# Optimization experiments

Hardware: AMD Instinct MI355X
Metric: run time of the kernel (lower is better)

Reference implementation:

```python
import jax, jax.numpy as jnp
import numpy as np

B, T, D, H = 4, 2048, 512, 8
K = D // H  # head dim = 64

def setup_inputs() -> dict:
    key = jax.random.key(0)
    k1, k2, k3, k4 = jax.random.split(key, 4)
    x = jax.random.normal(k1, (B, T, D), dtype=jnp.float32)
    # torch nn.Linear stores weight as [out_features, in_features]
    w_qkv = jax.random.normal(k2, (3 * D, D), dtype=jnp.float32) * (D ** -0.5)
    w_proj = jax.random.normal(k3, (D, D), dtype=jnp.float32) * (D ** -0.5)
    b_proj = jax.random.normal(k4, (D,), dtype=jnp.float32) * 0.01
    return {"x": x, "w_qkv": w_qkv, "w_proj": w_proj, "b_proj": b_proj}

def reference(x, w_qkv, w_proj, b_proj):
    Bx, Tx, Dx = x.shape
    # qkv projection (no bias): [B,T,3D]
    qkv = jnp.einsum('btd,ed->bte', x, w_qkv)
    q, k, v = jnp.split(qkv, 3, axis=-1)
    # [B,H,T,K]
    def heads(t):
        return t.reshape(Bx, Tx, H, K).transpose(0, 2, 1, 3)
    q, k, v = heads(q), heads(k), heads(v)
    # scaled scores with causal mask
    scores = jnp.einsum('bhqk,bhsk->bhqs', q, k) * (K ** -0.5)  # [B,H,T,T]
    causal = jnp.tril(jnp.ones((Tx, Tx), dtype=bool))
    scores = jnp.where(causal, scores, -jnp.inf)
    attn = jax.nn.softmax(scores, axis=-1)  # dropout p=0.0 -> identity
    out = jnp.einsum('bhqs,bhsk->bhqk', attn, v)  # [B,H,T,K]
    out = out.transpose(0, 2, 1, 3).reshape(Bx, Tx, Dx)
    out = jnp.einsum('btd,ed->bte', out, w_proj) + b_proj
    return out
```

## Files before the change

### kernel.cpp

```cpp
#include <hip/hip_runtime.h>
#include <hip/hip_bf16.h>


typedef unsigned short u16;
typedef __attribute__((ext_vector_type(8))) __bf16 bf16x8;
typedef __attribute__((ext_vector_type(8))) unsigned short u16x8;
typedef __attribute__((ext_vector_type(4))) unsigned short u16x4;
typedef __attribute__((ext_vector_type(4))) float f32x4;
typedef __attribute__((ext_vector_type(4))) unsigned u32x4;
typedef __attribute__((ext_vector_type(2))) unsigned u32x2;

#define DEV static __device__ __forceinline__

DEV void async16(const u16* g, u16* l) {
  __builtin_amdgcn_global_load_lds(
      (const __attribute__((address_space(1))) unsigned int*)g,
      (__attribute__((address_space(3))) unsigned int*)l, 16, 0, 0);
}
DEV u16x8 gld8(const u16* p) { return *(const u16x8*)p; }
DEV void lst8(u16* p, u16x8 v) { *(u16x8*)p = v; }
DEV bf16x8 ldsld8(const u16* p) {
  return __builtin_bit_cast(bf16x8, *(const u16x8*)p);
}
DEV f32x4 mfma16(bf16x8 a, bf16x8 b, f32x4 c) {
  return __builtin_amdgcn_mfma_f32_16x16x32_bf16(a, b, c, 0, 0, 0);
}
DEV u16 f2b(float f) {
  unsigned u = __builtin_bit_cast(unsigned, f);
  u += 0x7FFFu + ((u >> 16) & 1u);
  return (u16)(u >> 16);
}
DEV unsigned pk2(float x, float y) {
  __hip_bfloat162 t = __float22bfloat162_rn(float2{x, y});
  unsigned r;
  __builtin_memcpy(&r, &t, 4);
  return r;
}
DEV u16x8 pack8(f32x4 a, f32x4 b) {
  u32x4 t;
  t[0] = pk2(a[0], a[1]);
  t[1] = pk2(a[2], a[3]);
  t[2] = pk2(b[0], b[1]);
  t[3] = pk2(b[2], b[3]);
  return __builtin_bit_cast(u16x8, t);
}

__global__ void cvt_all(const float* __restrict__ x, const float* __restrict__ wq,
                        u16* __restrict__ xb, u16* __restrict__ wqb) {
  constexpr long NX = 8192L * 512 / 8;
  constexpr long NQ = 1536L * 512 / 8;
  const long i = (long)blockIdx.x * 256 + threadIdx.x;
  if (i < NX) {
    const float* p = x + i * 8;
    *(u16x8*)(xb + i * 8) = pack8(*(const f32x4*)p, *(const f32x4*)(p + 4));
  } else if (i < NX + NQ) {
    const long j = i - NX;
    const float* p = wq + j * 8;
    *(u16x8*)(wqb + j * 8) = pack8(*(const f32x4*)p, *(const f32x4*)(p + 4));
  }
}

__global__ void gemm_bb(const u16* __restrict__ A, const u16* __restrict__ Bt,
                        u16* __restrict__ qk, u16* __restrict__ vT, int K) {
  __shared__ __align__(16) u16 As[2][128 * 32];
  __shared__ __align__(16) u16 Bs[2][128 * 32];

  const int t = threadIdx.x, lane = t & 63, w = t >> 6;
  const int lane15 = lane & 15, quad = lane >> 4;
  const int wr = w >> 1, wc = w & 1;

  const int i = blockIdx.x;
  const int rt = (i & 7) | (((i >> 3) & 7) << 3);
  const int ct = i >> 6;
  const long row0 = (long)rt * 128;
  const int col0 = ct * 128;

  const int srow = w * 16 + (lane >> 2);
  const int scol = (lane & 3) * 8;
  const u16* Ag = A + (row0 + srow) * (long)K + scol;
  const u16* Bg = Bt + ((long)col0 + srow) * (long)K + scol;

  f32x4 acc[4][4];
#pragma unroll
  for (int ii = 0; ii < 4; ii++)
#pragma unroll
    for (int j = 0; j < 4; j++) acc[ii][j] = (f32x4)(0.0f);

  for (int k0 = 0; k0 < K; k0 += 64) {
    __syncthreads();
#pragma unroll
    for (int r = 0; r < 2; r++)
#pragma unroll
      for (int hf = 0; hf < 2; hf++) {
        async16(Ag + (long)r * 64 * K + k0 + hf * 32,
                &As[hf][(r * 64 + w * 16) * 32]);
        async16(Bg + (long)r * 64 * K + k0 + hf * 32,
                &Bs[hf][(r * 64 + w * 16) * 32]);
      }
    __syncthreads();

#pragma unroll
    for (int hf = 0; hf < 2; hf++) {
      bf16x8 a[4], b[4];
#pragma unroll
      for (int ii = 0; ii < 4; ii++)
        a[ii] = ldsld8(&As[hf][(wr * 64 + ii * 16 + lane15) * 32 + quad * 8]);
#pragma unroll
      for (int j = 0; j < 4; j++)
        b[j] = ldsld8(&Bs[hf][(wc * 64 + j * 16 + lane15) * 32 + quad * 8]);
#pragma unroll
      for (int ii = 0; ii < 4; ii++)
#pragma unroll
        for (int j = 0; j < 4; j++) acc[ii][j] = mfma16(a[ii], b[j], acc[ii][j]);
    }
  }

  if (col0 >= 1024) {
#pragma unroll
    for (int ii = 0; ii < 4; ii++)
#pragma unroll
      for (int j = 0; j < 4; j++) {
        const int hd = col0 - 1024 + wc * 64 + j * 16 + lane15;
        const long row = row0 + wr * 64 + ii * 16 + quad * 4;
        const long bb = row >> 11;
        const int s = (int)(row & 2047);
        const int ps = (s & ~31) | (((s >> 2) & 3) << 3) | (((s >> 4) & 1) << 2);
        u32x2 pr;
        pr[0] = pk2(acc[ii][j][0], acc[ii][j][1]);
        pr[1] = pk2(acc[ii][j][2], acc[ii][j][3]);
        *(u16x4*)(vT + (bb * 512 + hd) * 2048 + ps) =
            __builtin_bit_cast(u16x4, pr);
      }
  } else {
#pragma unroll
    for (int ii = 0; ii < 4; ii++)
#pragma unroll
      for (int j = 0; j < 4; j++) {
        const int col = col0 + wc * 64 + j * 16 + lane15;
        const float sc = (col < 512) ? 0.18033688f : 1.0f;
#pragma unroll
        for (int r = 0; r < 4; r++) {
          const long row = row0 + wr * 64 + ii * 16 + quad * 4 + r;
          qk[row * 1024 + col] = f2b(acc[ii][j][r] * sc);
        }
      }
  }
}

__global__ void gemm_b64(const u16* __restrict__ A, const float* __restrict__ Bt,
                         const float* __restrict__ bias, float* __restrict__ C,
                         int N, int K) {
  __shared__ __align__(16) u16 As[2][128 * 32];
  __shared__ __align__(16) u16 Bs[2][64 * 32];

  const int t = threadIdx.x, lane = t & 63, w = t >> 6;
  const int lane15 = lane & 15, quad = lane >> 4;
  const int wr = w >> 1, wc = w & 1;

  const int i = blockIdx.x;
  const int rt = (i & 7) | (((i >> 3) & 7) << 3);
  const int ct = i >> 6;
  const long row0 = (long)rt * 128;
  const int col0 = ct * 64;

  const int srow = w * 16 + (lane >> 2);
  const int scol = (lane & 3) * 8;
  const u16* Ag = A + (row0 + srow) * (long)K + scol;

  const int brow = t >> 2, bc = (t & 3) * 16;
  const float* Bg = Bt + (long)(col0 + brow) * K + bc;
  u16* BsD = &Bs[bc >> 5][brow * 32 + (bc & 31)];

  f32x4 acc[4][2];
#pragma unroll
  for (int ii = 0; ii < 4; ii++)
#pragma unroll
    for (int j = 0; j < 2; j++) acc[ii][j] = (f32x4)(0.0f);

  f32x4 q0 = *(const f32x4*)Bg, q1 = *(const f32x4*)(Bg + 4);
  f32x4 q2 = *(const f32x4*)(Bg + 8), q3 = *(const f32x4*)(Bg + 12);

  for (int k0 = 0; k0 < K; k0 += 64) {
    __syncthreads();
#pragma unroll
    for (int r = 0; r < 2; r++)
#pragma unroll
      for (int hf = 0; hf < 2; hf++)
        async16(Ag + (long)r * 64 * K + k0 + hf * 32,
                &As[hf][(r * 64 + w * 16) * 32]);
    lst8(BsD, pack8(q0, q1));
    lst8(BsD + 8, pack8(q2, q3));
    __syncthreads();

    {
      const int kp = (k0 + 64 < K) ? k0 + 64 : k0;
      q0 = *(const f32x4*)(Bg + kp);     q1 = *(const f32x4*)(Bg + kp + 4);
      q2 = *(const f32x4*)(Bg + kp + 8); q3 = *(const f32x4*)(Bg + kp + 12);
    }

#pragma unroll
    for (int hf = 0; hf < 2; hf++) {
      bf16x8 a[4], b[2];
#pragma unroll
      for (int ii = 0; ii < 4; ii++)
        a[ii] = ldsld8(&As[hf][(wr * 64 + ii * 16 + lane15) * 32 + quad * 8]);
#pragma unroll
      for (int j = 0; j < 2; j++)
        b[j] = ldsld8(&Bs[hf][(wc * 32 + j * 16 + lane15) * 32 + quad * 8]);
#pragma unroll
      for (int ii = 0; ii < 4; ii++)
#pragma unroll
        for (int j = 0; j < 2; j++) acc[ii][j] = mfma16(a[ii], b[j], acc[ii][j]);
    }
  }

#pragma unroll
  for (int ii = 0; ii < 4; ii++)
#pragma unroll
    for (int j = 0; j < 2; j++) {
      const int col = col0 + wc * 32 + j * 16 + lane15;
      const float bv = bias[col];
#pragma unroll
      for (int r = 0; r < 4; r++) {
        const long row = row0 + wr * 64 + ii * 16 + quad * 4 + r;
        C[row * (long)N + col] = acc[ii][j][r] + bv;
      }
    }
}

__global__ void attn_v8(const u16* __restrict__ qk, const u16* __restrict__ vT,
                        u16* __restrict__ out) {
  constexpr int T = 2048, LDQ = 1024;
  __shared__ __align__(16) u16 Ks[2][64 * 72];
  __shared__ __align__(16) u16 Vs[2][64 * 72];

  const int t = threadIdx.x, lane = t & 63, w = t >> 6;
  const int lane15 = lane & 15, quad = lane >> 4;

  const int i = blockIdx.x;
  int qb = i & 15;
  if (i >= 256) qb = 15 - qb;
  const int h = (i >> 4) & 7;
  const int b = (i >> 7) & 3;
  const long baseq = (long)b * T * LDQ;
  const u16* vTb = vT + ((long)b * 512 + h * 64) * 2048;

  const u16* gq =
      qk + baseq + (long)(qb * 128 + w * 32 + lane15) * LDQ + h * 64 + quad * 8;
  const bf16x8 qa0 = __builtin_bit_cast(bf16x8, *(const u16x8*)gq);
  const bf16x8 qa1 = __builtin_bit_cast(bf16x8, *(const u16x8*)(gq + 32));
  const bf16x8 qc0 = __builtin_bit_cast(bf16x8, *(const u16x8*)(gq + 16 * LDQ));
  const bf16x8 qc1 =
      __builtin_bit_cast(bf16x8, *(const u16x8*)(gq + 16 * LDQ + 32));

  const int srow = t >> 3, sc8 = (t & 7) * 8;
  const int nsb = 2 * qb + 2;
  const int sbd = 2 * qb + (w >> 1);

  const u16* gk = qk + baseq + (long)srow * LDQ + 512 + h * 64 + sc8;
  const u16* gv = vTb + (long)srow * 2048 + sc8;

  u16x8 kr0, kr1, vr0, vr1;
  kr0 = gld8(gk); kr1 = gld8(gk + (long)32 * LDQ);
  vr0 = gld8(gv); vr1 = gld8(gv + (long)32 * 2048);
  lst8(&Ks[0][srow * 72 + sc8], kr0);
  lst8(&Ks[0][(srow + 32) * 72 + sc8], kr1);
  lst8(&Vs[0][srow * 72 + sc8], vr0);
  lst8(&Vs[0][(srow + 32) * 72 + sc8], vr1);
  gk += (long)64 * LDQ;
  gv += 64;
  kr0 = gld8(gk); kr1 = gld8(gk + (long)32 * LDQ);
  vr0 = gld8(gv); vr1 = gld8(gv + (long)32 * 2048);

  f32x4 o0[4], o1[4], lsum0 = (f32x4)(0.0f), lsum1 = (f32x4)(0.0f);
#pragma unroll
  for (int j = 0; j < 4; j++) { o0[j] = (f32x4)(0.0f); o1[j] = (f32x4)(0.0f); }

  const bf16x8 ones = __builtin_bit_cast(bf16x8, (u16x8)((u16)0x3F80));
  const int ql0 = ((w & 1) << 5) + lane15;

  for (int sb = 0; sb < nsb; ++sb) {
    const u16* Kc = Ks[sb & 1];
    const u16* Vc = Vs[sb & 1];
    u16* Kn = Ks[(sb + 1) & 1];
    u16* Vn = Vs[(sb + 1) & 1];

    __syncthreads();

    lst8(&Kn[srow * 72 + sc8], kr0);
    lst8(&Kn[(srow + 32) * 72 + sc8], kr1);
    lst8(&Vn[srow * 72 + sc8], vr0);
    lst8(&Vn[(srow + 32) * 72 + sc8], vr1);

    if (sb + 2 < nsb) { gk += (long)64 * LDQ; gv += 64; }
    kr0 = gld8(gk); kr1 = gld8(gk + (long)32 * LDQ);
    vr0 = gld8(gv); vr1 = gld8(gv + (long)32 * 2048);

    if (sb <= sbd) {
      __builtin_amdgcn_s_setprio(1);
      f32x4 s0[4], s1[4];
#pragma unroll
      for (int j = 0; j < 4; j++) {
        const bf16x8 k0 = ldsld8(&Kc[(j * 16 + lane15) * 72 + quad * 8]);
        const bf16x8 k1 = ldsld8(&Kc[(j * 16 + lane15) * 72 + quad * 8 + 32]);
        s0[j] = mfma16(k1, qa1, mfma16(k0, qa0, (f32x4)(0.0f)));
        s1[j] = mfma16(k1, qc1, mfma16(k0, qc0, (f32x4)(0.0f)));
      }

#pragma unroll
      for (int j = 0; j < 4; j++)
#pragma unroll
        for (int r = 0; r < 4; r++) {
          s0[j][r] = exp2f(s0[j][r]);
          s1[j][r] = exp2f(s1[j][r]);
        }
      if (sb == sbd) {
#pragma unroll
        for (int j = 0; j < 4; j++)
#pragma unroll
          for (int r = 0; r < 4; r++) {
            const int sl = j * 16 + quad * 4 + r;
            if (sl > ql0) s0[j][r] = 0.0f;
            if (sl > ql0 + 16) s1[j][r] = 0.0f;
          }
      }

      u32x4 w0, w1, w2, w3;
      w0[0] = pk2(s0[0][0], s0[0][1]); w0[1] = pk2(s0[0][2], s0[0][3]);
      w0[2] = pk2(s0[1][0], s0[1][1]); w0[3] = pk2(s0[1][2], s0[1][3]);
      w1[0] = pk2(s0[2][0], s0[2][1]); w1[1] = pk2(s0[2][2], s0[2][3]);
      w1[2] = pk2(s0[3][0], s0[3][1]); w1[3] = pk2(s0[3][2], s0[3][3]);
      w2[0] = pk2(s1[0][0], s1[0][1]); w2[1] = pk2(s1[0][2], s1[0][3]);
      w2[2] = pk2(s1[1][0], s1[1][1]); w2[3] = pk2(s1[1][2], s1[1][3]);
      w3[0] = pk2(s1[2][0], s1[2][1]); w3[1] = pk2(s1[2][2], s1[2][3]);
      w3[2] = pk2(s1[3][0], s1[3][1]); w3[3] = pk2(s1[3][2], s1[3][3]);
      const bf16x8 pa0 = __builtin_bit_cast(bf16x8, w0);
      const bf16x8 pa1 = __builtin_bit_cast(bf16x8, w1);
      const bf16x8 pc0 = __builtin_bit_cast(bf16x8, w2);
      const bf16x8 pc1 = __builtin_bit_cast(bf16x8, w3);

#pragma unroll
      for (int j = 0; j < 4; j++) {
        const int d0 = (j * 16 + lane15) * 72;
        const bf16x8 v0 = ldsld8(&Vc[d0 + quad * 8]);
        const bf16x8 v1 = ldsld8(&Vc[d0 + quad * 8 + 32]);
        o0[j] = mfma16(pa1, v1, mfma16(pa0, v0, o0[j]));
        o1[j] = mfma16(pc1, v1, mfma16(pc0, v0, o1[j]));
      }
      lsum0 = mfma16(pa1, ones, mfma16(pa0, ones, lsum0));
      lsum1 = mfma16(pc1, ones, mfma16(pc0, ones, lsum1));
      __builtin_amdgcn_s_setprio(0);
    }
  }

  const long orow0 = (long)b * T + qb * 128 + w * 32;
  f32x4 inv0, inv1;
#pragma unroll
  for (int r = 0; r < 4; r++) {
    inv0[r] = 1.0f / lsum0[r];
    inv1[r] = 1.0f / lsum1[r];
  }
#pragma unroll
  for (int j = 0; j < 4; j++)
#pragma unroll
    for (int r = 0; r < 4; r++) {
      const long rr = orow0 + quad * 4 + r;
      out[rr * 512 + h * 64 + j * 16 + lane15] = f2b(o0[j][r] * inv0[r]);
      out[(rr + 16) * 512 + h * 64 + j * 16 + lane15] = f2b(o1[j][r] * inv1[r]);
    }
}

extern "C" void kernel_launch(void* const* d_in, const int* in_sizes, int n_in,
                              void* d_out, int out_size, void* d_ws, size_t ws_size,
                              hipStream_t stream) {
  const float* x      = (const float*)d_in[0];
  const float* w_qkv  = (const float*)d_in[1];
  const float* w_proj = (const float*)d_in[2];
  const float* b_proj = (const float*)d_in[3];
  float* out = (float*)d_out;

  u16* qk = (u16*)d_ws;
  u16* vT = qk + (size_t)8192 * 1024;
  u16* xb = vT + (size_t)4 * 512 * 2048;
  u16* wqb = (u16*)d_out;

  cvt_all<<<2432, 256, 0, stream>>>(x, w_qkv, xb, wqb);
  gemm_bb<<<768, 256, 0, stream>>>(xb, wqb, qk, vT, 512);
  attn_v8<<<512, 256, 0, stream>>>(qk, vT, xb);
  gemm_b64<<<512, 256, 0, stream>>>(xb, w_proj, b_proj, out, 512, 512);
}
```

Measured before the change: 153.7 us.

## Split attention key range across two wave-halves per block and combine via LDS

The attention kernel now launches 512 threads per block, with two groups of 4 waves. Each group processes half of the causal key blocks for the same 128 query rows using its own double-buffered K/V LDS tiles. At the end, the second group writes its unnormalized partial outputs and row sums to LDS, and the first group adds them, normalizes and stores. This is meant to shorten the serial per-block key loop and raise wave count for the long-causal blocks, at the cost of doubled LDS, an extra combine step, and block-wide syncs that now span both halves.

```diff
diff --git a/kernel.cpp b/kernel.cpp
--- a/kernel.cpp
+++ b/kernel.cpp
@@ -228,14 +228,16 @@
     }
 }
 
-__global__ void attn_v8(const u16* __restrict__ qk, const u16* __restrict__ vT,
-                        u16* __restrict__ out) {
+__global__ void __launch_bounds__(512, 4)
+attn_v9(const u16* __restrict__ qk, const u16* __restrict__ vT,
+        u16* __restrict__ out) {
   constexpr int T = 2048, LDQ = 1024;
-  __shared__ __align__(16) u16 Ks[2][64 * 72];
-  __shared__ __align__(16) u16 Vs[2][64 * 72];
+  __shared__ __align__(16) u16 Ks[2][2][64 * 72];
+  __shared__ __align__(16) u16 Vs[2][2][64 * 72];
 
   const int t = threadIdx.x, lane = t & 63, w = t >> 6;
   const int lane15 = lane & 15, quad = lane >> 4;
+  const int half = w >> 2, wl = w & 3;
 
   const int i = blockIdx.x;
   int qb = i & 15;
@@ -246,29 +248,30 @@
   const u16* vTb = vT + ((long)b * 512 + h * 64) * 2048;
 
   const u16* gq =
-      qk + baseq + (long)(qb * 128 + w * 32 + lane15) * LDQ + h * 64 + quad * 8;
+      qk + baseq + (long)(qb * 128 + wl * 32 + lane15) * LDQ + h * 64 + quad * 8;
   const bf16x8 qa0 = __builtin_bit_cast(bf16x8, *(const u16x8*)gq);
   const bf16x8 qa1 = __builtin_bit_cast(bf16x8, *(const u16x8*)(gq + 32));
   const bf16x8 qc0 = __builtin_bit_cast(bf16x8, *(const u16x8*)(gq + 16 * LDQ));
   const bf16x8 qc1 =
       __builtin_bit_cast(bf16x8, *(const u16x8*)(gq + 16 * LDQ + 32));
 
-  const int srow = t >> 3, sc8 = (t & 7) * 8;
-  const int nsb = 2 * qb + 2;
-  const int sbd = 2 * qb + (w >> 1);
-
-  const u16* gk = qk + baseq + (long)srow * LDQ + 512 + h * 64 + sc8;
-  const u16* gv = vTb + (long)srow * 2048 + sc8;
+  const int th = t & 255;
+  const int srow = th >> 3, sc8 = (th & 7) * 8;
+  const int nsbh = qb + 1;
+  const int s0 = half * nsbh;
+  const int sbd = 2 * qb + (wl >> 1);
+
+  const u16* gk = qk + baseq + (long)(s0 * 64 + srow) * LDQ + 512 + h * 64 + sc8;
+  const u16* gv = vTb + (long)srow * 2048 + s0 * 64 + sc8;
 
   u16x8 kr0, kr1, vr0, vr1;
   kr0 = gld8(gk); kr1 = gld8(gk + (long)32 * LDQ);
   vr0 = gld8(gv); vr1 = gld8(gv + (long)32 * 2048);
-  lst8(&Ks[0][srow * 72 + sc8], kr0);
-  lst8(&Ks[0][(srow + 32) * 72 + sc8], kr1);
-  lst8(&Vs[0][srow * 72 + sc8], vr0);
-  lst8(&Vs[0][(srow + 32) * 72 + sc8], vr1);
-  gk += (long)64 * LDQ;
-  gv += 64;
+  lst8(&Ks[half][0][srow * 72 + sc8], kr0);
+  lst8(&Ks[half][0][(srow + 32) * 72 + sc8], kr1);
+  lst8(&Vs[half][0][srow * 72 + sc8], vr0);
+  lst8(&Vs[half][0][(srow + 32) * 72 + sc8], vr1);
+  if (nsbh > 1) { gk += (long)64 * LDQ; gv += 64; }
   kr0 = gld8(gk); kr1 = gld8(gk + (long)32 * LDQ);
   vr0 = gld8(gv); vr1 = gld8(gv + (long)32 * 2048);
 
@@ -277,13 +280,13 @@
   for (int j = 0; j < 4; j++) { o0[j] = (f32x4)(0.0f); o1[j] = (f32x4)(0.0f); }
 
   const bf16x8 ones = __builtin_bit_cast(bf16x8, (u16x8)((u16)0x3F80));
-  const int ql0 = ((w & 1) << 5) + lane15;
-
-  for (int sb = 0; sb < nsb; ++sb) {
-    const u16* Kc = Ks[sb & 1];
-    const u16* Vc = Vs[sb & 1];
-    u16* Kn = Ks[(sb + 1) & 1];
-    u16* Vn = Vs[(sb + 1) & 1];
+  const int ql0 = ((wl & 1) << 5) + lane15;
+
+  for (int it = 0; it < nsbh; ++it) {
+    const u16* Kc = Ks[half][it & 1];
+    const u16* Vc = Vs[half][it & 1];
+    u16* Kn = Ks[half][(it + 1) & 1];
+    u16* Vn = Vs[half][(it + 1) & 1];
 
     __syncthreads();
 
@@ -292,27 +295,28 @@
     lst8(&Vn[srow * 72 + sc8], vr0);
     lst8(&Vn[(srow + 32) * 72 + sc8], vr1);
 
-    if (sb + 2 < nsb) { gk += (long)64 * LDQ; gv += 64; }
+    if (it + 2 < nsbh) { gk += (long)64 * LDQ; gv += 64; }
     kr0 = gld8(gk); kr1 = gld8(gk + (long)32 * LDQ);
     vr0 = gld8(gv); vr1 = gld8(gv + (long)32 * 2048);
 
+    const int sb = s0 + it;
     if (sb <= sbd) {
       __builtin_amdgcn_s_setprio(1);
-      f32x4 s0[4], s1[4];
+      f32x4 sf0[4], sf1[4];
 #pragma unroll
       for (int j = 0; j < 4; j++) {
         const bf16x8 k0 = ldsld8(&Kc[(j * 16 + lane15) * 72 + quad * 8]);
         const bf16x8 k1 = ldsld8(&Kc[(j * 16 + lane15) * 72 + quad * 8 + 32]);
-        s0[j] = mfma16(k1, qa1, mfma16(k0, qa0, (f32x4)(0.0f)));
-        s1[j] = mfma16(k1, qc1, mfma16(k0, qc0, (f32x4)(0.0f)));
+        sf0[j] = mfma16(k1, qa1, mfma16(k0, qa0, (f32x4)(0.0f)));
+        sf1[j] = mfma16(k1, qc1, mfma16(k0, qc0, (f32x4)(0.0f)));
       }
 
 #pragma unroll
       for (int j = 0; j < 4; j++)
 #pragma unroll
         for (int r = 0; r < 4; r++) {
-          s0[j][r] = exp2f(s0[j][r]);
-          s1[j][r] = exp2f(s1[j][r]);
+          sf0[j][r] = exp2f(sf0[j][r]);
+          sf1[j][r] = exp2f(sf1[j][r]);
         }
       if (sb == sbd) {
 #pragma unroll
@@ -320,20 +324,20 @@
 #pragma unroll
           for (int r = 0; r < 4; r++) {
             const int sl = j * 16 + quad * 4 + r;
-            if (sl > ql0) s0[j][r] = 0.0f;
-            if (sl > ql0 + 16) s1[j][r] = 0.0f;
+            if (sl > ql0) sf0[j][r] = 0.0f;
+            if (sl > ql0 + 16) sf1[j][r] = 0.0f;
           }
       }
 
       u32x4 w0, w1, w2, w3;
-      w0[0] = pk2(s0[0][0], s0[0][1]); w0[1] = pk2(s0[0][2], s0[0][3]);
-      w0[2] = pk2(s0[1][0], s0[1][1]); w0[3] = pk2(s0[1][2], s0[1][3]);
-      w1[0] = pk2(s0[2][0], s0[2][1]); w1[1] = pk2(s0[2][2], s0[2][3]);
-      w1[2] = pk2(s0[3][0], s0[3][1]); w1[3] = pk2(s0[3][2], s0[3][3]);
-      w2[0] = pk2(s1[0][0], s1[0][1]); w2[1] = pk2(s1[0][2], s1[0][3]);
-      w2[2] = pk2(s1[1][0], s1[1][1]); w2[3] = pk2(s1[1][2], s1[1][3]);
-      w3[0] = pk2(s1[2][0], s1[2][1]); w3[1] = pk2(s1[2][2], s1[2][3]);
-      w3[2] = pk2(s1[3][0], s1[3][1]); w3[3] = pk2(s1[3][2], s1[3][3]);
+      w0[0] = pk2(sf0[0][0], sf0[0][1]); w0[1] = pk2(sf0[0][2], sf0[0][3]);
+      w0[2] = pk2(sf0[1][0], sf0[1][1]); w0[3] = pk2(sf0[1][2], sf0[1][3]);
+      w1[0] = pk2(sf0[2][0], sf0[2][1]); w1[1] = pk2(sf0[2][2], sf0[2][3]);
+      w1[2] = pk2(sf0[3][0], sf0[3][1]); w1[3] = pk2(sf0[3][2], sf0[3][3]);
+      w2[0] = pk2(sf1[0][0], sf1[0][1]); w2[1] = pk2(sf1[0][2], sf1[0][3]);
+      w2[2] = pk2(sf1[1][0], sf1[1][1]); w2[3] = pk2(sf1[1][2], sf1[1][3]);
+      w3[0] = pk2(sf1[2][0], sf1[2][1]); w3[1] = pk2(sf1[2][2], sf1[2][3]);
+      w3[2] = pk2(sf1[3][0], sf1[3][1]); w3[3] = pk2(sf1[3][2], sf1[3][3]);
       const bf16x8 pa0 = __builtin_bit_cast(bf16x8, w0);
       const bf16x8 pa1 = __builtin_bit_cast(bf16x8, w1);
       const bf16x8 pc0 = __builtin_bit_cast(bf16x8, w2);
@@ -353,21 +357,49 @@
     }
   }
 
-  const long orow0 = (long)b * T + qb * 128 + w * 32;
-  f32x4 inv0, inv1;
-#pragma unroll
-  for (int r = 0; r < 4; r++) {
-    inv0[r] = 1.0f / lsum0[r];
-    inv1[r] = 1.0f / lsum1[r];
-  }
-#pragma unroll
-  for (int j = 0; j < 4; j++)
+  __syncthreads();
+  float* cmb = (float*)&Ks[0][0][0];
+  float* cl = (float*)&Vs[0][0][0];
+
+  if (half == 1) {
+    const int q0 = wl * 32 + quad * 4;
+#pragma unroll
+    for (int j = 0; j < 4; j++)
+#pragma unroll
+      for (int r = 0; r < 4; r++) {
+        cmb[(q0 + r) * 64 + j * 16 + lane15] = o0[j][r];
+        cmb[(q0 + 16 + r) * 64 + j * 16 + lane15] = o1[j][r];
+      }
+    if (lane15 == 0) {
+#pragma unroll
+      for (int r = 0; r < 4; r++) {
+        cl[q0 + r] = lsum0[r];
+        cl[q0 + 16 + r] = lsum1[r];
+      }
+    }
+  }
+  __syncthreads();
+
+  if (half == 0) {
+    const int q0 = wl * 32 + quad * 4;
+    f32x4 inv0, inv1;
 #pragma unroll
     for (int r = 0; r < 4; r++) {
-      const long rr = orow0 + quad * 4 + r;
-      out[rr * 512 + h * 64 + j * 16 + lane15] = f2b(o0[j][r] * inv0[r]);
-      out[(rr + 16) * 512 + h * 64 + j * 16 + lane15] = f2b(o1[j][r] * inv1[r]);
-    }
+      inv0[r] = 1.0f / (lsum0[r] + cl[q0 + r]);
+      inv1[r] = 1.0f / (lsum1[r] + cl[q0 + 16 + r]);
+    }
+    const long orow0 = (long)b * T + qb * 128 + wl * 32;
+#pragma unroll
+    for (int j = 0; j < 4; j++)
+#pragma unroll
+      for (int r = 0; r < 4; r++) {
+        const float a0 = o0[j][r] + cmb[(q0 + r) * 64 + j * 16 + lane15];
+        const float a1 = o1[j][r] + cmb[(q0 + 16 + r) * 64 + j * 16 + lane15];
+        const long rr = orow0 + quad * 4 + r;
+        out[rr * 512 + h * 64 + j * 16 + lane15] = f2b(a0 * inv0[r]);
+        out[(rr + 16) * 512 + h * 64 + j * 16 + lane15] = f2b(a1 * inv1[r]);
+      }
+  }
 }
 
 extern "C" void kernel_launch(void* const* d_in, const int* in_sizes, int n_in,
@@ -386,6 +418,6 @@
 
   cvt_all<<<2432, 256, 0, stream>>>(x, w_qkv, xb, wqb);
   gemm_bb<<<768, 256, 0, stream>>>(xb, wqb, qk, vT, 512);
-  attn_v8<<<512, 256, 0, stream>>>(qk, vT, xb);
+  attn_v9<<<512, 512, 0, stream>>>(qk, vT, xb);
   gemm_b64<<<512, 256, 0, stream>>>(xb, w_proj, b_proj, out, 512, 512);
 }
```

Result: faster. 146.9 us (-4.4%).
